# Kernel tuning notes

Measured on AMD Instinct MI355X. Metric: run time of the kernel, lower is better.

The kernel has to match this reference:

```python
import jax, jax.numpy as jnp
import numpy as np

EMBED_DIM = 1024
NUM_HEADS = 16
HEAD_DIM = EMBED_DIM // NUM_HEADS


def setup_inputs() -> dict:
    key = jax.random.key(0)
    ks = jax.random.split(key, 10)
    s = 1.0 / np.sqrt(EMBED_DIM)
    x = jax.random.normal(ks[0], (2, 2048, EMBED_DIM), dtype=jnp.float32)
    Wq = jax.random.uniform(ks[1], (EMBED_DIM, EMBED_DIM), jnp.float32, -s, s)
    bq = jax.random.uniform(ks[2], (EMBED_DIM,), jnp.float32, -s, s)
    Wk = jax.random.uniform(ks[3], (EMBED_DIM, EMBED_DIM), jnp.float32, -s, s)
    bk = jax.random.uniform(ks[4], (EMBED_DIM,), jnp.float32, -s, s)
    Wv = jax.random.uniform(ks[5], (EMBED_DIM, EMBED_DIM), jnp.float32, -s, s)
    bv = jax.random.uniform(ks[6], (EMBED_DIM,), jnp.float32, -s, s)
    Wo = jax.random.uniform(ks[7], (EMBED_DIM, EMBED_DIM), jnp.float32, -s, s)
    bo = jax.random.uniform(ks[8], (EMBED_DIM,), jnp.float32, -s, s)
    return {"x": x, "Wq": Wq, "bq": bq, "Wk": Wk, "bk": bk,
            "Wv": Wv, "bv": bv, "Wo": Wo, "bo": bo}


def reference(x, Wq, bq, Wk, bk, Wv, bv, Wo, bo):
    b, s, e = x.shape
    h, d = NUM_HEADS, HEAD_DIM
    scale = d ** -0.5
    # projections (torch Linear: x @ W.T + b; here W stored as [in, out])
    q = (x @ Wq + bq).reshape(b, s, h, d)
    k = (x @ Wk + bk).reshape(b, s, h, d)
    v = (x @ Wv + bv).reshape(b, s, h, d)
    logits = jnp.einsum('bqhd,bkhd->bhqk', q, k) * scale
    causal = jnp.tril(jnp.ones((s, s), dtype=bool))  # keep lower triangle
    logits = jnp.where(causal, logits, -jnp.inf)
    attn = jax.nn.softmax(logits, axis=-1)
    out = jnp.einsum('bhqk,bkhd->bqhd', attn, v).reshape(b, s, e)
    return out @ Wo + bo
```

## Files before the change

### kernel.cpp

```cpp
#include <hip/hip_runtime.h>


#define EMB 1024
#define SEQ 2048
#define NB 2
#define NH 16
#define HD 64

#define QSCALE 0.18033688011112042f

typedef float f32x4 __attribute__((ext_vector_type(4)));
typedef float floatx4 __attribute__((ext_vector_type(4)));
typedef short short8 __attribute__((ext_vector_type(8)));
typedef __bf16 bf16x8 __attribute__((ext_vector_type(8)));
typedef __bf16 bf16x2 __attribute__((ext_vector_type(2)));
typedef unsigned short ushortx4 __attribute__((ext_vector_type(4)));
typedef unsigned int uintx4 __attribute__((ext_vector_type(4)));

__device__ __forceinline__ unsigned short bf16u(float f) {
  __bf16 h = (__bf16)f;
  return __builtin_bit_cast(unsigned short, h);
}

__device__ __forceinline__ unsigned pkbf(float lo, float hi) {
  bf16x2 v;
  v[0] = (__bf16)lo;
  v[1] = (__bf16)hi;
  return __builtin_bit_cast(unsigned, v);
}

__device__ __forceinline__ f32x4 mfma16(short8 a, short8 b, f32x4 c) {
  return __builtin_amdgcn_mfma_f32_16x16x32_bf16(
      __builtin_bit_cast(bf16x8, a), __builtin_bit_cast(bf16x8, b), c, 0, 0, 0);
}

__device__ __forceinline__ void gload16(const void* g, void* lds) {
  __builtin_amdgcn_global_load_lds(
      (const __attribute__((address_space(1))) unsigned int*)g,
      (__attribute__((address_space(3))) unsigned int*)lds, 16, 0, 0);
}

__global__ __launch_bounds__(256) void cvt_x_kernel(
    const float* __restrict__ x, unsigned short* __restrict__ out) {
  const int idx = (blockIdx.x * 256 + threadIdx.x) * 4;
  floatx4 v = *(const floatx4*)(x + idx);
  ushortx4 o;
  #pragma unroll
  for (int i = 0; i < 4; ++i) o[i] = bf16u(v[i]);
  *(ushortx4*)(out + idx) = o;
}

__global__ __launch_bounds__(256) void cvt_w4_kernel(
    const float* __restrict__ W0, const float* __restrict__ W1,
    const float* __restrict__ W2, const float* __restrict__ W3,
    unsigned short* __restrict__ T0, unsigned short* __restrict__ T1,
    unsigned short* __restrict__ T2, unsigned short* __restrict__ T3) {
  __shared__ unsigned short tile[32][33];
  const int z = blockIdx.z;
  const float* W = (z == 0) ? W0 : (z == 1) ? W1 : (z == 2) ? W2 : W3;
  unsigned short* WT = (z == 0) ? T0 : (z == 1) ? T1 : (z == 2) ? T2 : T3;
  const int k0 = blockIdx.x * 32, n0 = blockIdx.y * 32;
  const int t = threadIdx.x;
  const int r = t >> 3, c = (t & 7) * 4;
  floatx4 v = *(const floatx4*)(W + (k0 + r) * EMB + n0 + c);
  #pragma unroll
  for (int i = 0; i < 4; ++i) tile[r][c + i] = bf16u(v[i]);
  __syncthreads();
  ushortx4 o;
  #pragma unroll
  for (int i = 0; i < 4; ++i) o[i] = tile[c + i][r];
  *(ushortx4*)(WT + (n0 + r) * EMB + k0 + c) = o;
}

#define GEMM_KLOOP(OP1, OP2)                                                 \
    for (int kk = 0; kk < 64; kk += 32) {                                    \
      short8 a[4], b[4];                                                     \
      _Pragma("unroll")                                                      \
      for (int i = 0; i < 4; ++i)                                            \
        a[i] = *(const short8*)(As + (wr * 64 + i * 16 + ln) * 64 + kk + g * 8); \
      _Pragma("unroll")                                                      \
      for (int j = 0; j < 4; ++j)                                            \
        b[j] = *(const short8*)(Bs + (wc * 64 + j * 16 + ln) * 64 + kk + g * 8); \
      _Pragma("unroll")                                                      \
      for (int i = 0; i < 4; ++i)                                            \
        _Pragma("unroll")                                                    \
        for (int j = 0; j < 4; ++j)                                          \
          acc[i][j] = mfma16(OP1, OP2, acc[i][j]);                           \
    }

#define GEMM_STAGE(Aptr, Bptr, kt_, buf_)                                    \
    do {                                                                     \
      const int kb_ = (kt_) * 64;                                            \
      _Pragma("unroll")                                                      \
      for (int it = 0; it < 4; ++it) {                                       \
        const int chunk = w * 4 + it;                                        \
        const int lin = chunk * 64 + l;                                      \
        const int row = lin >> 3, col = (lin & 7) * 8;                       \
        gload16(Aptr + (m0 + row) * EMB + kb_ + col,                         \
                (char*)&AsB[buf_][0] + chunk * 1024);                        \
        gload16(Bptr + (n0 + row) * EMB + kb_ + col,                         \
                (char*)&BsB[buf_][0] + chunk * 1024);                        \
      }                                                                      \
    } while (0)

__global__ __launch_bounds__(256) void gemm_qkv_kernel(
    const unsigned short* __restrict__ Xb,
    const unsigned short* __restrict__ W0, const unsigned short* __restrict__ W1,
    const unsigned short* __restrict__ W2,
    const float* __restrict__ b0, const float* __restrict__ b1,
    const float* __restrict__ b2,
    unsigned short* __restrict__ Qo, unsigned short* __restrict__ Ko,
    unsigned short* __restrict__ Vo) {
  __shared__ __align__(16) unsigned short AsB[2][128 * 64];
  __shared__ __align__(16) unsigned short BsB[2][128 * 64];
  const int z = blockIdx.z;
  const unsigned short* Wt = (z == 0) ? W0 : ((z == 1) ? W1 : W2);
  const float* bias = (z == 0) ? b0 : ((z == 1) ? b1 : b2);
  const bool sw = (z != 2);
  const int m0 = blockIdx.y * 128, n0 = blockIdx.x * 128;
  const int tid = threadIdx.x, l = tid & 63, w = tid >> 6;
  const int g = l >> 4, ln = l & 15;
  const int wr = w >> 1, wc = w & 1;

  f32x4 acc[4][4];
  #pragma unroll
  for (int i = 0; i < 4; ++i)
    #pragma unroll
    for (int j = 0; j < 4; ++j) acc[i][j] = (f32x4){0.f, 0.f, 0.f, 0.f};

  GEMM_STAGE(Xb, Wt, 0, 0);
  #pragma unroll 1
  for (int kt = 0; kt < 16; ++kt) {
    const int cur = kt & 1;
    if (kt + 1 < 16) {
      GEMM_STAGE(Xb, Wt, kt + 1, cur ^ 1);
      asm volatile("s_waitcnt vmcnt(8)" ::: "memory");
    } else {
      asm volatile("s_waitcnt vmcnt(0)" ::: "memory");
    }
    __builtin_amdgcn_s_barrier();
    const unsigned short* As = &AsB[cur][0];
    const unsigned short* Bs = &BsB[cur][0];
    if (sw) {
      GEMM_KLOOP(b[j], a[i])
    } else {
      GEMM_KLOOP(a[i], b[j])
    }
    asm volatile("" ::: "memory");
    __builtin_amdgcn_s_barrier();
  }

  const int mb = m0 + wr * 64, nb = n0 + wc * 64;
  if (sw) {
    unsigned short* dst = (z == 0) ? Qo : Ko;
    const float osc = (z == 0) ? QSCALE : 1.0f;
    #pragma unroll
    for (int j = 0; j < 4; ++j) {
      const int n = nb + j * 16 + 4 * g;
      floatx4 bv_ = *(const floatx4*)(bias + n);
      const int h = n >> 6, d = n & 63;
      #pragma unroll
      for (int i = 0; i < 4; ++i) {
        const int m = mb + i * 16 + ln;
        const int bb = m >> 11, ss = m & 2047;
        ushortx4 o;
        #pragma unroll
        for (int e = 0; e < 4; ++e) o[e] = bf16u((acc[i][j][e] + bv_[e]) * osc);
        *(ushortx4*)(dst + ((bb * NH + h) * SEQ + ss) * HD + d) = o;
      }
    }
  } else {
    #pragma unroll
    for (int j = 0; j < 4; ++j) {
      const int n = nb + j * 16 + ln;
      const float bgain = bias[n];
      const int h = n >> 6, d = n & 63;
      #pragma unroll
      for (int i = 0; i < 4; ++i) {
        const int mf = mb + i * 16 + 4 * g;
        const int bb = mf >> 11, ss = mf & 2047;
        ushortx4 o;
        #pragma unroll
        for (int e = 0; e < 4; ++e) o[e] = bf16u(acc[i][j][e] + bgain);
        *(ushortx4*)(Vo + ((bb * NH + h) * HD + d) * SEQ + ss) = o;
      }
    }
  }
}

__global__ __launch_bounds__(512) void attn_kernel(
    const unsigned short* __restrict__ Q, const unsigned short* __restrict__ K,
    const unsigned short* __restrict__ Vt, unsigned short* __restrict__ O) {
  __shared__ __align__(16) unsigned short Kt[2][128 * 64];
  __shared__ __align__(16) unsigned short Vl[2][64 * 128];
  const int id = blockIdx.x;
  const int bh = id & 31;
  const int grp = id >> 5;
  const int T = (grp < 8) ? (15 - grp) : (grp - 8);
  const int h = bh & 15, b = bh >> 4;
  const int tid = threadIdx.x, l = tid & 63, w = tid >> 6;
  const int g = l >> 4, ln = l & 15;
  const size_t baseQK = (size_t)bh * SEQ * HD;
  const size_t baseV = (size_t)bh * HD * SEQ;
  const int xr = ln & 7;
  const int srcA = ((g & 1) << 5) + ln;
  const int srcB = srcA + 16;
  const bool hi = (g >> 1) != 0;

  const int kr0 = (2 * w) * 8 + (l >> 3), kr1 = (2 * w + 1) * 8 + (l >> 3);
  const int kc0 = (l & 7) ^ (kr0 & 7), kc1 = (l & 7) ^ (kr1 & 7);
  const int vr0 = (2 * w) * 4 + (l >> 4), vr1 = (2 * w + 1) * 4 + (l >> 4);
  const int vc0 = (l & 15) ^ (vr0 & 15), vc1 = (l & 15) ^ (vr1 & 15);

  const int nkt = T + 1;
  const int qw = T * 128 + w * 16;

  gload16(K + baseQK + (size_t)kr0 * HD + kc0 * 8,
          (char*)&Kt[0][0] + (2 * w) * 1024);
  gload16(K + baseQK + (size_t)kr1 * HD + kc1 * 8,
          (char*)&Kt[0][0] + (2 * w + 1) * 1024);
  gload16(Vt + baseV + (size_t)vr0 * SEQ + vc0 * 8,
          (char*)&Vl[0][0] + (2 * w) * 1024);
  gload16(Vt + baseV + (size_t)vr1 * SEQ + vc1 * 8,
          (char*)&Vl[0][0] + (2 * w + 1) * 1024);

  const int qrow = qw + ln;
  short8 qf0 = *(const short8*)(Q + baseQK + (size_t)qrow * HD + g * 8);
  short8 qf1 = *(const short8*)(Q + baseQK + (size_t)qrow * HD + 32 + g * 8);

  float m_run = -1e30f, l_run = 0.f;
  f32x4 acc[4];
  #pragma unroll
  for (int dj = 0; dj < 4; ++dj) acc[dj] = (f32x4){0.f, 0.f, 0.f, 0.f};

  #pragma unroll 1
  for (int kt = 0; kt < nkt; ++kt) {
    const int cur = kt & 1;
    const bool has_next = (kt + 1 < nkt);
    if (has_next) {
      const int nxt = cur ^ 1;
      const size_t kof = (size_t)(kt + 1) * 128;
      gload16(K + baseQK + (kof + kr0) * HD + kc0 * 8,
              (char*)&Kt[nxt][0] + (2 * w) * 1024);
      gload16(K + baseQK + (kof + kr1) * HD + kc1 * 8,
              (char*)&Kt[nxt][0] + (2 * w + 1) * 1024);
      gload16(Vt + baseV + (size_t)vr0 * SEQ + kof + vc0 * 8,
              (char*)&Vl[nxt][0] + (2 * w) * 1024);
      gload16(Vt + baseV + (size_t)vr1 * SEQ + kof + vc1 * 8,
              (char*)&Vl[nxt][0] + (2 * w + 1) * 1024);
      asm volatile("s_waitcnt vmcnt(4)" ::: "memory");
    } else {
      asm volatile("s_waitcnt vmcnt(0)" ::: "memory");
    }
    __builtin_amdgcn_s_barrier();

    const bool last = (kt == T);
    const int jmax = last ? w : 7;

    f32x4 sv[8];
    #pragma unroll
    for (int j = 0; j < 8; ++j)
      sv[j] = (f32x4){-1e30f, -1e30f, -1e30f, -1e30f};
    __builtin_amdgcn_s_setprio(1);
    #pragma unroll
    for (int j = 0; j < 8; ++j) {
      if (j <= jmax) {
        f32x4 t = (f32x4){0.f, 0.f, 0.f, 0.f};
        short8 kf0 = *(const short8*)(
            &Kt[cur][(j * 16 + ln) * 64 + ((g ^ xr) * 8)]);
        t = mfma16(kf0, qf0, t);
        short8 kf1 = *(const short8*)(
            &Kt[cur][(j * 16 + ln) * 64 + (((4 + g) ^ xr) * 8)]);
        t = mfma16(kf1, qf1, t);
        if (last && j == w) {
          #pragma unroll
          for (int e = 0; e < 4; ++e)
            sv[j][e] = (4 * g + e <= ln) ? t[e] : -1e30f;
        } else {
          sv[j] = t;
        }
      }
    }
    __builtin_amdgcn_s_setprio(0);

    float tj[8];
    #pragma unroll
    for (int j = 0; j < 8; ++j)
      tj[j] = fmaxf(fmaxf(sv[j][0], sv[j][1]), fmaxf(sv[j][2], sv[j][3]));
    float tm = fmaxf(fmaxf(fmaxf(tj[0], tj[1]), fmaxf(tj[2], tj[3])),
                     fmaxf(fmaxf(tj[4], tj[5]), fmaxf(tj[6], tj[7])));
    tm = fmaxf(tm, __shfl_xor(tm, 16));
    tm = fmaxf(tm, __shfl_xor(tm, 32));
    const float nm = fmaxf(m_run, tm);
    const float al = exp2f(m_run - nm);
    m_run = nm;

    unsigned pk[8][2];
    float rs = 0.f;
    #pragma unroll
    for (int j = 0; j < 8; ++j) {
      const float p0 = exp2f(sv[j][0] - nm), p1 = exp2f(sv[j][1] - nm);
      const float p2 = exp2f(sv[j][2] - nm), p3 = exp2f(sv[j][3] - nm);
      rs += (p0 + p1) + (p2 + p3);
      pk[j][0] = pkbf(p0, p1);
      pk[j][1] = pkbf(p2, p3);
    }
    rs += __shfl_xor(rs, 16);
    rs += __shfl_xor(rs, 32);
    l_run = l_run * al + rs;
    #pragma unroll
    for (int dj = 0; dj < 4; ++dj) acc[dj] *= al;

    const int ksmax = (jmax >> 1) + 1;
    short8 pf[4];
    #pragma unroll
    for (int ks = 0; ks < 4; ++ks) {
      if (ks < ksmax) {
        unsigned a0 = __shfl(pk[2 * ks][0], srcA);
        unsigned a1 = __shfl(pk[2 * ks][1], srcA);
        unsigned a2 = __shfl(pk[2 * ks][0], srcB);
        unsigned a3 = __shfl(pk[2 * ks][1], srcB);
        unsigned b0 = __shfl(pk[2 * ks + 1][0], srcA);
        unsigned b1 = __shfl(pk[2 * ks + 1][1], srcA);
        unsigned b2 = __shfl(pk[2 * ks + 1][0], srcB);
        unsigned b3 = __shfl(pk[2 * ks + 1][1], srcB);
        uintx4 u;
        u[0] = hi ? b0 : a0; u[1] = hi ? b1 : a1;
        u[2] = hi ? b2 : a2; u[3] = hi ? b3 : a3;
        pf[ks] = __builtin_bit_cast(short8, u);
      }
    }

    __builtin_amdgcn_s_setprio(1);
    #pragma unroll
    for (int dj = 0; dj < 4; ++dj) {
      #pragma unroll
      for (int ks = 0; ks < 4; ++ks) {
        if (ks < ksmax) {
          short8 vb = *(const short8*)(
              &Vl[cur][(dj * 16 + ln) * 128 + (((ks * 4 + g) ^ ln) * 8)]);
          acc[dj] = mfma16(vb, pf[ks], acc[dj]);
        }
      }
    }
    __builtin_amdgcn_s_setprio(0);

    asm volatile("" ::: "memory");
    __builtin_amdgcn_s_barrier();
  }

  const float inv = 1.f / l_run;
  const size_t orow = ((size_t)b * SEQ + qw + ln) * EMB + h * HD;
  #pragma unroll
  for (int dj = 0; dj < 4; ++dj) {
    ushortx4 o;
    #pragma unroll
    for (int e = 0; e < 4; ++e) o[e] = bf16u(acc[dj][e] * inv);
    *(ushortx4*)(O + orow + dj * 16 + 4 * g) = o;
  }
}

__global__ __launch_bounds__(256) void gemm_o_kernel(
    const unsigned short* __restrict__ Ab, const unsigned short* __restrict__ Wt,
    const float* __restrict__ bias, float* __restrict__ out) {
  __shared__ __align__(16) unsigned short AsB[2][128 * 64];
  __shared__ __align__(16) unsigned short BsB[2][128 * 64];
  const int m0 = blockIdx.y * 128, n0 = blockIdx.x * 128;
  const int tid = threadIdx.x, l = tid & 63, w = tid >> 6;
  const int g = l >> 4, ln = l & 15;
  const int wr = w >> 1, wc = w & 1;

  f32x4 acc[4][4];
  #pragma unroll
  for (int i = 0; i < 4; ++i)
    #pragma unroll
    for (int j = 0; j < 4; ++j) acc[i][j] = (f32x4){0.f, 0.f, 0.f, 0.f};

  GEMM_STAGE(Ab, Wt, 0, 0);
  #pragma unroll 1
  for (int kt = 0; kt < 16; ++kt) {
    const int cur = kt & 1;
    if (kt + 1 < 16) {
      GEMM_STAGE(Ab, Wt, kt + 1, cur ^ 1);
      asm volatile("s_waitcnt vmcnt(8)" ::: "memory");
    } else {
      asm volatile("s_waitcnt vmcnt(0)" ::: "memory");
    }
    __builtin_amdgcn_s_barrier();
    const unsigned short* As = &AsB[cur][0];
    const unsigned short* Bs = &BsB[cur][0];
    GEMM_KLOOP(b[j], a[i])
    asm volatile("" ::: "memory");
    __builtin_amdgcn_s_barrier();
  }

  const int mb = m0 + wr * 64, nb = n0 + wc * 64;
  #pragma unroll
  for (int j = 0; j < 4; ++j) {
    const int n = nb + j * 16 + 4 * g;
    floatx4 bv_ = *(const floatx4*)(bias + n);
    #pragma unroll
    for (int i = 0; i < 4; ++i) {
      const int m = mb + i * 16 + ln;
      floatx4 o = acc[i][j] + bv_;
      *(floatx4*)(out + (size_t)m * EMB + n) = o;
    }
  }
}

extern "C" void kernel_launch(void* const* d_in, const int* in_sizes, int n_in,
                              void* d_out, int out_size, void* d_ws, size_t ws_size,
                              hipStream_t stream) {
  const float* x  = (const float*)d_in[0];
  const float* Wq = (const float*)d_in[1];
  const float* bq = (const float*)d_in[2];
  const float* Wk = (const float*)d_in[3];
  const float* bk = (const float*)d_in[4];
  const float* Wv = (const float*)d_in[5];
  const float* bv = (const float*)d_in[6];
  const float* Wo = (const float*)d_in[7];
  const float* bo = (const float*)d_in[8];
  float* out = (float*)d_out;

  char* ws = (char*)d_ws;
  unsigned short* Xb  = (unsigned short*)(ws);
  unsigned short* WqT = (unsigned short*)(ws + 8388608);
  unsigned short* WkT = (unsigned short*)(ws + 10485760);
  unsigned short* WvT = (unsigned short*)(ws + 12582912);
  unsigned short* WoT = (unsigned short*)(ws + 14680064);
  unsigned short* Qb  = (unsigned short*)(ws + 16777216);
  unsigned short* Kb  = (unsigned short*)(ws + 25165824);
  unsigned short* Vtb = (unsigned short*)(ws + 33554432);
  unsigned short* Ao  = Xb;

  hipLaunchKernelGGL(cvt_x_kernel, dim3(4096), dim3(256), 0, stream, x, Xb);
  hipLaunchKernelGGL(cvt_w4_kernel, dim3(32, 32, 4), dim3(256), 0, stream,
                     Wq, Wk, Wv, Wo, WqT, WkT, WvT, WoT);
  hipLaunchKernelGGL(gemm_qkv_kernel, dim3(8, 32, 3), dim3(256), 0, stream,
                     Xb, WqT, WkT, WvT, bq, bk, bv, Qb, Kb, Vtb);
  hipLaunchKernelGGL(attn_kernel, dim3(512), dim3(512), 0, stream,
                     Qb, Kb, Vtb, Ao);
  hipLaunchKernelGGL(gemm_o_kernel, dim3(8, 32), dim3(256), 0, stream,
                     Ao, WoT, bo, out);
}
```

Measured before the change: 161.7 us.

## Switch attention to 32x32x16 MFMA with four 32-row waves per block

Rewrites the attention kernel to use 32x32x16 bf16 MFMA tiles. Each of four waves now handles 32 query rows, where before eight waves each handled 16. The P matrix is rearranged for the PV product with permlane32_swap instead of many cross-lane shuffles, and each wave issues more K/V loads. This cuts shuffle overhead and raises MFMA size per LDS read, at the cost of fewer waves per block for latency hiding, more registers, and scalar 2-byte output stores.

```diff
diff --git a/kernel.cpp b/kernel.cpp
--- a/kernel.cpp
+++ b/kernel.cpp
@@ -10,12 +10,14 @@
 #define QSCALE 0.18033688011112042f
 
 typedef float f32x4 __attribute__((ext_vector_type(4)));
+typedef float f32x16 __attribute__((ext_vector_type(16)));
 typedef float floatx4 __attribute__((ext_vector_type(4)));
 typedef short short8 __attribute__((ext_vector_type(8)));
 typedef __bf16 bf16x8 __attribute__((ext_vector_type(8)));
 typedef __bf16 bf16x2 __attribute__((ext_vector_type(2)));
 typedef unsigned short ushortx4 __attribute__((ext_vector_type(4)));
 typedef unsigned int uintx4 __attribute__((ext_vector_type(4)));
+typedef int int2v __attribute__((ext_vector_type(2)));
 
 __device__ __forceinline__ unsigned short bf16u(float f) {
   __bf16 h = (__bf16)f;
@@ -32,6 +34,17 @@
 __device__ __forceinline__ f32x4 mfma16(short8 a, short8 b, f32x4 c) {
   return __builtin_amdgcn_mfma_f32_16x16x32_bf16(
       __builtin_bit_cast(bf16x8, a), __builtin_bit_cast(bf16x8, b), c, 0, 0, 0);
+}
+
+__device__ __forceinline__ f32x16 mfma32(short8 a, short8 b, f32x16 c) {
+  return __builtin_amdgcn_mfma_f32_32x32x16_bf16(
+      __builtin_bit_cast(bf16x8, a), __builtin_bit_cast(bf16x8, b), c, 0, 0, 0);
+}
+
+__device__ __forceinline__ void plswap(unsigned& a, unsigned& b) {
+  int2v r = __builtin_amdgcn_permlane32_swap((int)a, (int)b, false, false);
+  a = (unsigned)r[0];
+  b = (unsigned)r[1];
 }
 
 __device__ __forceinline__ void gload16(const void* g, void* lds) {
@@ -188,7 +201,7 @@
   }
 }
 
-__global__ __launch_bounds__(512) void attn_kernel(
+__global__ __launch_bounds__(256) void attn_kernel(
     const unsigned short* __restrict__ Q, const unsigned short* __restrict__ K,
     const unsigned short* __restrict__ Vt, unsigned short* __restrict__ O) {
   __shared__ __align__(16) unsigned short Kt[2][128 * 64];
@@ -199,39 +212,41 @@
   const int T = (grp < 8) ? (15 - grp) : (grp - 8);
   const int h = bh & 15, b = bh >> 4;
   const int tid = threadIdx.x, l = tid & 63, w = tid >> 6;
-  const int g = l >> 4, ln = l & 15;
+  const int q32 = l & 31;
+  const int hi = l >> 5;
   const size_t baseQK = (size_t)bh * SEQ * HD;
   const size_t baseV = (size_t)bh * HD * SEQ;
-  const int xr = ln & 7;
-  const int srcA = ((g & 1) << 5) + ln;
-  const int srcB = srcA + 16;
-  const bool hi = (g >> 1) != 0;
-
-  const int kr0 = (2 * w) * 8 + (l >> 3), kr1 = (2 * w + 1) * 8 + (l >> 3);
-  const int kc0 = (l & 7) ^ (kr0 & 7), kc1 = (l & 7) ^ (kr1 & 7);
-  const int vr0 = (2 * w) * 4 + (l >> 4), vr1 = (2 * w + 1) * 4 + (l >> 4);
-  const int vc0 = (l & 15) ^ (vr0 & 15), vc1 = (l & 15) ^ (vr1 & 15);
+
+  const int krw = l >> 3;
+  const int kcg = (l & 7) ^ (l >> 3);
+  const int vrw = l >> 4;
 
   const int nkt = T + 1;
-  const int qw = T * 128 + w * 16;
-
-  gload16(K + baseQK + (size_t)kr0 * HD + kc0 * 8,
-          (char*)&Kt[0][0] + (2 * w) * 1024);
-  gload16(K + baseQK + (size_t)kr1 * HD + kc1 * 8,
-          (char*)&Kt[0][0] + (2 * w + 1) * 1024);
-  gload16(Vt + baseV + (size_t)vr0 * SEQ + vc0 * 8,
-          (char*)&Vl[0][0] + (2 * w) * 1024);
-  gload16(Vt + baseV + (size_t)vr1 * SEQ + vc1 * 8,
-          (char*)&Vl[0][0] + (2 * w + 1) * 1024);
-
-  const int qrow = qw + ln;
-  short8 qf0 = *(const short8*)(Q + baseQK + (size_t)qrow * HD + g * 8);
-  short8 qf1 = *(const short8*)(Q + baseQK + (size_t)qrow * HD + 32 + g * 8);
+  const int qw = T * 128 + w * 32;
+
+  #pragma unroll
+  for (int i = 0; i < 4; ++i) {
+    const int c = 4 * w + i;
+    gload16(K + baseQK + (size_t)(8 * c + krw) * HD + kcg * 8,
+            (char*)&Kt[0][0] + c * 1024);
+    const int vr = 4 * c + vrw;
+    const int vcg = (l & 15) ^ (vr & 15);
+    gload16(Vt + baseV + (size_t)vr * SEQ + vcg * 8,
+            (char*)&Vl[0][0] + c * 1024);
+  }
+
+  const int qrow = qw + q32;
+  short8 qf[4];
+  #pragma unroll
+  for (int ds = 0; ds < 4; ++ds)
+    qf[ds] = *(const short8*)(Q + baseQK + (size_t)qrow * HD + ds * 16 + hi * 8);
 
   float m_run = -1e30f, l_run = 0.f;
-  f32x4 acc[4];
-  #pragma unroll
-  for (int dj = 0; dj < 4; ++dj) acc[dj] = (f32x4){0.f, 0.f, 0.f, 0.f};
+  f32x16 acc[2];
+  #pragma unroll
+  for (int dh = 0; dh < 2; ++dh)
+    #pragma unroll
+    for (int r = 0; r < 16; ++r) acc[dh][r] = 0.f;
 
   #pragma unroll 1
   for (int kt = 0; kt < nkt; ++kt) {
@@ -240,106 +255,118 @@
     if (has_next) {
       const int nxt = cur ^ 1;
       const size_t kof = (size_t)(kt + 1) * 128;
-      gload16(K + baseQK + (kof + kr0) * HD + kc0 * 8,
-              (char*)&Kt[nxt][0] + (2 * w) * 1024);
-      gload16(K + baseQK + (kof + kr1) * HD + kc1 * 8,
-              (char*)&Kt[nxt][0] + (2 * w + 1) * 1024);
-      gload16(Vt + baseV + (size_t)vr0 * SEQ + kof + vc0 * 8,
-              (char*)&Vl[nxt][0] + (2 * w) * 1024);
-      gload16(Vt + baseV + (size_t)vr1 * SEQ + kof + vc1 * 8,
-              (char*)&Vl[nxt][0] + (2 * w + 1) * 1024);
-      asm volatile("s_waitcnt vmcnt(4)" ::: "memory");
+      #pragma unroll
+      for (int i = 0; i < 4; ++i) {
+        const int c = 4 * w + i;
+        gload16(K + baseQK + (kof + 8 * c + krw) * HD + kcg * 8,
+                (char*)&Kt[nxt][0] + c * 1024);
+        const int vr = 4 * c + vrw;
+        const int vcg = (l & 15) ^ (vr & 15);
+        gload16(Vt + baseV + (size_t)vr * SEQ + kof + vcg * 8,
+                (char*)&Vl[nxt][0] + c * 1024);
+      }
+      asm volatile("s_waitcnt vmcnt(8)" ::: "memory");
     } else {
       asm volatile("s_waitcnt vmcnt(0)" ::: "memory");
     }
     __builtin_amdgcn_s_barrier();
 
     const bool last = (kt == T);
-    const int jmax = last ? w : 7;
-
-    f32x4 sv[8];
-    #pragma unroll
-    for (int j = 0; j < 8; ++j)
-      sv[j] = (f32x4){-1e30f, -1e30f, -1e30f, -1e30f};
+
+    f32x16 sv[4];
+    #pragma unroll
+    for (int kj = 0; kj < 4; ++kj)
+      #pragma unroll
+      for (int r = 0; r < 16; ++r) sv[kj][r] = -1e30f;
+
     __builtin_amdgcn_s_setprio(1);
     #pragma unroll
-    for (int j = 0; j < 8; ++j) {
-      if (j <= jmax) {
-        f32x4 t = (f32x4){0.f, 0.f, 0.f, 0.f};
-        short8 kf0 = *(const short8*)(
-            &Kt[cur][(j * 16 + ln) * 64 + ((g ^ xr) * 8)]);
-        t = mfma16(kf0, qf0, t);
-        short8 kf1 = *(const short8*)(
-            &Kt[cur][(j * 16 + ln) * 64 + (((4 + g) ^ xr) * 8)]);
-        t = mfma16(kf1, qf1, t);
-        if (last && j == w) {
+    for (int kj = 0; kj < 4; ++kj) {
+      if (!last || kj <= w) {
+        f32x16 t;
+        #pragma unroll
+        for (int r = 0; r < 16; ++r) t[r] = 0.f;
+        #pragma unroll
+        for (int ds = 0; ds < 4; ++ds) {
+          short8 kf = *(const short8*)(
+              &Kt[cur][(kj * 32 + q32) * 64 + (((ds * 2 + hi) ^ (l & 7)) * 8)]);
+          t = mfma32(kf, qf[ds], t);
+        }
+        if (last && kj == w) {
           #pragma unroll
-          for (int e = 0; e < 4; ++e)
-            sv[j][e] = (4 * g + e <= ln) ? t[e] : -1e30f;
+          for (int r = 0; r < 16; ++r) {
+            const int crow = (r & 3) + 8 * (r >> 2) + 4 * hi;
+            sv[kj][r] = (crow <= q32) ? t[r] : -1e30f;
+          }
         } else {
-          sv[j] = t;
+          sv[kj] = t;
         }
       }
     }
     __builtin_amdgcn_s_setprio(0);
 
-    float tj[8];
-    #pragma unroll
-    for (int j = 0; j < 8; ++j)
-      tj[j] = fmaxf(fmaxf(sv[j][0], sv[j][1]), fmaxf(sv[j][2], sv[j][3]));
-    float tm = fmaxf(fmaxf(fmaxf(tj[0], tj[1]), fmaxf(tj[2], tj[3])),
-                     fmaxf(fmaxf(tj[4], tj[5]), fmaxf(tj[6], tj[7])));
-    tm = fmaxf(tm, __shfl_xor(tm, 16));
+    float tm = -1e30f;
+    #pragma unroll
+    for (int kj = 0; kj < 4; ++kj)
+      #pragma unroll
+      for (int r = 0; r < 16; ++r) tm = fmaxf(tm, sv[kj][r]);
     tm = fmaxf(tm, __shfl_xor(tm, 32));
     const float nm = fmaxf(m_run, tm);
     const float al = exp2f(m_run - nm);
     m_run = nm;
 
-    unsigned pk[8][2];
+    #pragma unroll
+    for (int r = 0; r < 16; ++r) {
+      const int crb = (r & 3) + 8 * (r >> 2);
+      const float ar = __shfl(al, crb + 4 * hi);
+      acc[0][r] *= ar;
+      acc[1][r] *= ar;
+    }
+
     float rs = 0.f;
-    #pragma unroll
-    for (int j = 0; j < 8; ++j) {
-      const float p0 = exp2f(sv[j][0] - nm), p1 = exp2f(sv[j][1] - nm);
-      const float p2 = exp2f(sv[j][2] - nm), p3 = exp2f(sv[j][3] - nm);
-      rs += (p0 + p1) + (p2 + p3);
-      pk[j][0] = pkbf(p0, p1);
-      pk[j][1] = pkbf(p2, p3);
-    }
-    rs += __shfl_xor(rs, 16);
+    short8 pa[8];
+    #pragma unroll
+    for (int kj = 0; kj < 4; ++kj) {
+      if (!last || kj <= w) {
+        float p[16];
+        #pragma unroll
+        for (int r = 0; r < 16; ++r) {
+          p[r] = exp2f(sv[kj][r] - nm);
+          rs += p[r];
+        }
+        unsigned A0 = pkbf(p[0], p[1]);
+        unsigned B0 = pkbf(p[2], p[3]);
+        unsigned C0 = pkbf(p[4], p[5]);
+        unsigned D0 = pkbf(p[6], p[7]);
+        plswap(A0, C0);
+        plswap(B0, D0);
+        uintx4 u0;
+        u0[0] = A0; u0[1] = B0; u0[2] = C0; u0[3] = D0;
+        pa[2 * kj] = __builtin_bit_cast(short8, u0);
+        unsigned A1 = pkbf(p[8], p[9]);
+        unsigned B1 = pkbf(p[10], p[11]);
+        unsigned C1 = pkbf(p[12], p[13]);
+        unsigned D1 = pkbf(p[14], p[15]);
+        plswap(A1, C1);
+        plswap(B1, D1);
+        uintx4 u1;
+        u1[0] = A1; u1[1] = B1; u1[2] = C1; u1[3] = D1;
+        pa[2 * kj + 1] = __builtin_bit_cast(short8, u1);
+      }
+    }
     rs += __shfl_xor(rs, 32);
     l_run = l_run * al + rs;
-    #pragma unroll
-    for (int dj = 0; dj < 4; ++dj) acc[dj] *= al;
-
-    const int ksmax = (jmax >> 1) + 1;
-    short8 pf[4];
-    #pragma unroll
-    for (int ks = 0; ks < 4; ++ks) {
-      if (ks < ksmax) {
-        unsigned a0 = __shfl(pk[2 * ks][0], srcA);
-        unsigned a1 = __shfl(pk[2 * ks][1], srcA);
-        unsigned a2 = __shfl(pk[2 * ks][0], srcB);
-        unsigned a3 = __shfl(pk[2 * ks][1], srcB);
-        unsigned b0 = __shfl(pk[2 * ks + 1][0], srcA);
-        unsigned b1 = __shfl(pk[2 * ks + 1][1], srcA);
-        unsigned b2 = __shfl(pk[2 * ks + 1][0], srcB);
-        unsigned b3 = __shfl(pk[2 * ks + 1][1], srcB);
-        uintx4 u;
-        u[0] = hi ? b0 : a0; u[1] = hi ? b1 : a1;
-        u[2] = hi ? b2 : a2; u[3] = hi ? b3 : a3;
-        pf[ks] = __builtin_bit_cast(short8, u);
-      }
-    }
-
+
+    const int smax = last ? (2 * w + 2) : 8;
     __builtin_amdgcn_s_setprio(1);
     #pragma unroll
-    for (int dj = 0; dj < 4; ++dj) {
-      #pragma unroll
-      for (int ks = 0; ks < 4; ++ks) {
-        if (ks < ksmax) {
+    for (int dh = 0; dh < 2; ++dh) {
+      #pragma unroll
+      for (int s = 0; s < 8; ++s) {
+        if (s < smax) {
           short8 vb = *(const short8*)(
-              &Vl[cur][(dj * 16 + ln) * 128 + (((ks * 4 + g) ^ ln) * 8)]);
-          acc[dj] = mfma16(vb, pf[ks], acc[dj]);
+              &Vl[cur][(32 * dh + q32) * 128 + (((s * 2 + hi) ^ (l & 15)) * 8)]);
+          acc[dh] = mfma32(pa[s], vb, acc[dh]);
         }
       }
     }
@@ -350,13 +377,16 @@
   }
 
   const float inv = 1.f / l_run;
-  const size_t orow = ((size_t)b * SEQ + qw + ln) * EMB + h * HD;
-  #pragma unroll
-  for (int dj = 0; dj < 4; ++dj) {
-    ushortx4 o;
-    #pragma unroll
-    for (int e = 0; e < 4; ++e) o[e] = bf16u(acc[dj][e] * inv);
-    *(ushortx4*)(O + orow + dj * 16 + 4 * g) = o;
+  #pragma unroll
+  for (int dh = 0; dh < 2; ++dh) {
+    #pragma unroll
+    for (int r = 0; r < 16; ++r) {
+      const int crb = (r & 3) + 8 * (r >> 2);
+      const float ir = __shfl(inv, crb + 4 * hi);
+      const int q = qw + crb + 4 * hi;
+      O[((size_t)b * SEQ + q) * EMB + h * HD + 32 * dh + q32] =
+          bf16u(acc[dh][r] * ir);
+    }
   }
 }
 
@@ -438,7 +468,7 @@
                      Wq, Wk, Wv, Wo, WqT, WkT, WvT, WoT);
   hipLaunchKernelGGL(gemm_qkv_kernel, dim3(8, 32, 3), dim3(256), 0, stream,
                      Xb, WqT, WkT, WvT, bq, bk, bv, Qb, Kb, Vtb);
-  hipLaunchKernelGGL(attn_kernel, dim3(512), dim3(512), 0, stream,
+  hipLaunchKernelGGL(attn_kernel, dim3(512), dim3(256), 0, stream,
                      Qb, Kb, Vtb, Ao);
   hipLaunchKernelGGL(gemm_o_kernel, dim3(8, 32), dim3(256), 0, stream,
                      Ao, WoT, bo, out);
```

After: 173.4 us. 1.07x slower.
